# Kernel optimization log

Measured on AMD Instinct MI355X. Metric: run time of the kernel, lower is better.

Reference implementation:

```python
import jax, jax.numpy as jnp
import numpy as np

BN_EPS = 1e-5
STRIDE = 4
K_NEAREST = 16


def _fps(xyz, m):
    """Farthest point sampling. xyz: [n,3] -> indices [m] (seeded at point 0)."""
    n = xyz.shape[0]

    def body(i, state):
        dist, idxs, last = state
        d = jnp.sum((xyz - xyz[last]) ** 2, axis=-1)
        dist = jnp.minimum(dist, d)
        nxt = jnp.argmax(dist).astype(jnp.int32)
        return dist, idxs.at[i].set(nxt), nxt

    init = (jnp.full((n,), 1e10, xyz.dtype), jnp.zeros((m,), jnp.int32), jnp.int32(0))
    _, idxs, _ = jax.lax.fori_loop(1, m, body, init)
    return idxs


def _knn(q, x, k):
    """q: [m,3] queries, x: [n,3] points -> [m,k] nearest-neighbor indices."""
    d = jnp.sum((q[:, None, :] - x[None, :, :]) ** 2, axis=-1)  # [m,n]
    _, idx = jax.lax.top_k(-d, k)
    return idx


def setup_inputs() -> dict:
    key = jax.random.key(0)
    k0, k1, k2 = jax.random.split(key, 3)
    B, N, IN_CH, OUT_CH = 4, 8192, 64, 128
    events = jax.random.uniform(k0, (B, N, 4), dtype=jnp.float32)  # xyz in [0,1) + time
    features = jax.random.normal(k1, (B, N, IN_CH), dtype=jnp.float32)
    W = jax.random.normal(k2, (4 + IN_CH, OUT_CH), dtype=jnp.float32) / np.float32(np.sqrt(4 + IN_CH))
    b = jnp.zeros((OUT_CH,), jnp.float32)
    gamma = jnp.ones((OUT_CH,), jnp.float32)
    beta = jnp.zeros((OUT_CH,), jnp.float32)
    return dict(events=events, features=features, W=W, b=b, gamma=gamma, beta=beta)


def reference(events, features, W, b, gamma, beta):
    B, N, _ = events.shape
    m = N // STRIDE  # down_offsets = offsets // stride with equal-size samples
    xyz = events[..., :3]
    xyz_c = jax.lax.stop_gradient(xyz)  # indices are non-differentiable

    # farthest point sampling per cloud -> [B, m]
    down_idx = jax.vmap(lambda p: _fps(p, m))(xyz_c)
    down_xyz = jnp.take_along_axis(xyz_c, down_idx[..., None], axis=1)  # [B,m,3]
    # k nearest neighbors of each sampled point -> [B, m, K]
    idx = jax.vmap(lambda q, x: _knn(q, x, K_NEAREST))(down_xyz, xyz_c)

    down_events = jnp.take_along_axis(events, down_idx[..., None], axis=1)  # [B,m,4]
    grouped_events = jax.vmap(lambda e, i: e[i])(events, idx)               # [B,m,K,4]
    grouped_events_norm = grouped_events - down_events[:, :, None, :]
    grouped_features = jax.vmap(lambda f, i: f[i])(features, idx)           # [B,m,K,in_ch]
    g = jnp.concatenate([grouped_events_norm, grouped_features], axis=-1)   # [B,m,K,4+in_ch]

    # Linear -> BatchNorm1d (training batch stats over all points & neighbors) -> ReLU
    h = jnp.einsum('bmkc,cd->bmkd', g, W) + b
    mu = jnp.mean(h, axis=(0, 1, 2))
    var = jnp.var(h, axis=(0, 1, 2))
    h = (h - mu) * jax.lax.rsqrt(var + BN_EPS) * gamma + beta
    h = jax.nn.relu(h)

    down_features = jnp.max(h, axis=2)  # max-pool over K neighbors -> [B,m,out_ch]
    return down_events, down_features
```

## Files before the change

### kernel.cpp

```cpp
#include <hip/hip_runtime.h>

#define N_PTS 8192
#define M_PTS 2048
#define K_NN 16
#define IN_CH 64
#define G_CH 68
#define OUT_CH 128
#define KCAP 128

__device__ __forceinline__ float subrn(float a, float b) {
    float r; asm("v_sub_f32 %0, %1, %2" : "=v"(r) : "v"(a), "v"(b)); return r;
}
__device__ __forceinline__ float mulrn(float a, float b) {
    float r; asm("v_mul_f32 %0, %1, %2" : "=v"(r) : "v"(a), "v"(b)); return r;
}
__device__ __forceinline__ float addrn(float a, float b) {
    float r; asm("v_add_f32 %0, %1, %2" : "=v"(r) : "v"(a), "v"(b)); return r;
}
__device__ __forceinline__ float sqdist_rn(float ax, float ay, float az,
                                           float bx, float by, float bz) {
    float dx = subrn(ax, bx);
    float dy = subrn(ay, by);
    float dz = subrn(az, bz);
    return addrn(addrn(mulrn(dx, dx), mulrn(dy, dy)), mulrn(dz, dz));
}

typedef float v2f __attribute__((ext_vector_type(2)));
__device__ __forceinline__ v2f pk_add(v2f a, v2f b) {
    v2f r; asm("v_pk_add_f32 %0, %1, %2" : "=v"(r) : "v"(a), "v"(b)); return r;
}
__device__ __forceinline__ v2f pk_mul(v2f a, v2f b) {
    v2f r; asm("v_pk_mul_f32 %0, %1, %2" : "=v"(r) : "v"(a), "v"(b)); return r;
}

template <int CTRL>
__device__ __forceinline__ float movdpp_f(float x) {
    int r = __builtin_amdgcn_mov_dpp(__float_as_int(x), CTRL, 0xf, 0xf, true);
    return __int_as_float(r);
}
template <int CTRL>
__device__ __forceinline__ int movdpp_i(int x) {
    return __builtin_amdgcn_mov_dpp(x, CTRL, 0xf, 0xf, true);
}
template <int CTRL, int RM>
__device__ __forceinline__ float dppmaxf_m(float x) {
    int r = __builtin_amdgcn_update_dpp(0, __float_as_int(x), CTRL, RM, 0xf, false);
    return fmaxf(x, __int_as_float(r));
}
__device__ __forceinline__ float wave_max64(float x) {
    x = fmaxf(x, movdpp_f<0xB1>(x));
    x = fmaxf(x, movdpp_f<0x4E>(x));
    x = fmaxf(x, movdpp_f<0x141>(x));
    x = fmaxf(x, movdpp_f<0x140>(x));
    x = dppmaxf_m<0x142, 0xa>(x);
    x = dppmaxf_m<0x143, 0xc>(x);
    return x;
}
__device__ __forceinline__ float group8_max(float x) {
    x = fmaxf(x, movdpp_f<0xB1>(x));
    x = fmaxf(x, movdpp_f<0x4E>(x));
    x = fmaxf(x, movdpp_f<0x141>(x));
    return x;
}
__device__ __forceinline__ int group8_min_i(int x) {
    x = min(x, movdpp_i<0xB1>(x));
    x = min(x, movdpp_i<0x4E>(x));
    x = min(x, movdpp_i<0x141>(x));
    return x;
}

__global__ __launch_bounds__(512) void fps_kernel(const float4* __restrict__ events4,
                                                  int* __restrict__ down_idx,
                                                  float4* __restrict__ out_de) {
    extern __shared__ char smem[];
    float*  rv   = (float*)smem;
    int*    wsl  = (int*)(smem + 32);
    int*    ssel = (int*)(smem + 64);
    float4* spt  = (float4*)(smem + 64 + 4 * M_PTS);

    const int b = blockIdx.x;
    const int tid = threadIdx.x;
    const int wave = tid >> 6;
    const int lane = tid & 63;
    const float4* ev = events4 + (size_t)b * N_PTS;

    for (int i = tid; i < N_PTS; i += 512) spt[i] = ev[i];
    if (tid == 0) ssel[0] = 0;
    __syncthreads();

    v2f px[8], py[8], pz[8];
    float dist[16];
#pragma unroll
    for (int pp = 0; pp < 8; ++pp) {
        float4 f0 = spt[tid * 16 + 2 * pp];
        float4 f1 = spt[tid * 16 + 2 * pp + 1];
        px[pp] = (v2f){f0.x, f1.x};
        py[pp] = (v2f){f0.y, f1.y};
        pz[pp] = (v2f){f0.z, f1.z};
        dist[2 * pp] = 1e10f; dist[2 * pp + 1] = 1e10f;
    }

    int last = 0;
    for (int i = 1; i < M_PTS; ++i) {
        float4 L = spt[last];
        const float nlx = -L.x, nly = -L.y, nlz = -L.z;
        const v2f nx2 = (v2f){nlx, nlx};
        const v2f ny2 = (v2f){nly, nly};
        const v2f nz2 = (v2f){nlz, nlz};
#pragma unroll
        for (int pp = 0; pp < 8; ++pp) {
            v2f dx = pk_add(px[pp], nx2);
            v2f dy = pk_add(py[pp], ny2);
            v2f dz = pk_add(pz[pp], nz2);
            v2f s  = pk_add(pk_add(pk_mul(dx, dx), pk_mul(dy, dy)), pk_mul(dz, dz));
            dist[2 * pp]     = fminf(dist[2 * pp],     s.x);
            dist[2 * pp + 1] = fminf(dist[2 * pp + 1], s.y);
        }
        float m0 = fmaxf(dist[0], dist[1]),  m1 = fmaxf(dist[2], dist[3]);
        float m2 = fmaxf(dist[4], dist[5]),  m3 = fmaxf(dist[6], dist[7]);
        float m4 = fmaxf(dist[8], dist[9]),  m5 = fmaxf(dist[10], dist[11]);
        float m6 = fmaxf(dist[12], dist[13]), m7 = fmaxf(dist[14], dist[15]);
        m0 = fmaxf(m0, m1); m2 = fmaxf(m2, m3); m4 = fmaxf(m4, m5); m6 = fmaxf(m6, m7);
        float bd = fmaxf(fmaxf(m0, m2), fmaxf(m4, m6));

        float wm = wave_max64(bd);
        if (lane == 63) rv[wave] = wm;
        __syncthreads();
        float bm = group8_max(rv[lane & 7]);

        bool cand = (bd == bm);
        unsigned long long mask = __ballot(cand);
        if (lane == 0) wsl[wave] = 0x7fffffff;
        if (mask != 0ULL) {
            int fl = (int)__ffsll((long long)mask) - 1;
            if (lane == fl) {
                int jm = 0;
#pragma unroll
                for (int j = 15; j >= 0; --j) if (dist[j] == bd) jm = j;
                wsl[wave] = tid * 16 + jm;
            }
        }
        __syncthreads();
        int winner = group8_min_i(wsl[lane & 7]);
        if (tid == 0) ssel[i] = winner;
        last = winner;
    }
    __syncthreads();

    for (int i = tid; i < M_PTS; i += 512) {
        int s = ssel[i];
        down_idx[b * M_PTS + i] = s;
        out_de[(size_t)b * M_PTS + i] = spt[s];
    }
}

__global__ __launch_bounds__(256) void knn_kernel(const float4* __restrict__ events4,
                                                  const int* __restrict__ down_idx,
                                                  int* __restrict__ knn_idx) {
    extern __shared__ char smem[];
    float* sx   = (float*)smem;
    float* sy   = sx + N_PTS;
    float* sz   = sy + N_PTS;
    float* cd   = sz + N_PTS;
    int*   ci   = (int*)(cd + 32 * KCAP);
    int*   scnt = (int*)(ci + 32 * KCAP);

    const int b    = blockIdx.x >> 6;
    const int qg   = blockIdx.x & 63;
    const int tid  = threadIdx.x;
    const int ql   = tid >> 3;
    const int part = tid & 7;

    const float4* ev = events4 + (size_t)b * N_PTS;
    for (int i = tid; i < N_PTS; i += 256) {
        float4 e = ev[i];
        sx[i] = e.x; sy[i] = e.y; sz[i] = e.z;
    }
    if (tid < 32) scnt[tid] = 0;
    __syncthreads();

    const int q  = qg * 32 + ql;
    const int qi = down_idx[b * M_PTS + q];
    const float qx = sx[qi], qy = sy[qi], qz = sz[qi];

    float m1 = 1e30f, m2 = 1e30f;
    for (int i = 0; i < N_PTS / 8; ++i) {
        const int p = i * 8 + part;
        float d = sqdist_rn(sx[p], sy[p], sz[p], qx, qy, qz);
        float lo = fminf(m1, d);
        m2 = fminf(m2, fmaxf(m1, d));
        m1 = lo;
    }
    const float T = group8_max(m2);

    for (int i = 0; i < N_PTS / 8; ++i) {
        const int p = i * 8 + part;
        float d = sqdist_rn(sx[p], sy[p], sz[p], qx, qy, qz);
        if (d <= T) {
            int pos = atomicAdd(&scnt[ql], 1);
            if (pos < KCAP) { cd[ql * KCAP + pos] = d; ci[ql * KCAP + pos] = p; }
        }
    }
    __syncthreads();

    if (part == 0) {
        float nd[16]; int ni[16];
#pragma unroll
        for (int j = 0; j < 16; ++j) { nd[j] = 1e30f; ni[j] = 0x7fffffff; }
        float wmax = 1e30f; int widx = 0x7fffffff; int wslot = 0;
        const int n = scnt[ql];
        const int lim = (n <= KCAP) ? n : 0;
        for (int t = 0; t < lim; ++t) {
            float d = cd[ql * KCAP + t];
            int   p = ci[ql * KCAP + t];
            if (d < wmax || (d == wmax && p < widx)) {
#pragma unroll
                for (int j = 0; j < 16; ++j) if (j == wslot) { nd[j] = d; ni[j] = p; }
                float m_ = -1.0f; int mix_ = -1; int ms_ = 0;
#pragma unroll
                for (int j = 0; j < 16; ++j)
                    if (nd[j] > m_ || (nd[j] == m_ && ni[j] > mix_)) { m_ = nd[j]; mix_ = ni[j]; ms_ = j; }
                wmax = m_; widx = mix_; wslot = ms_;
            }
        }
        if (n > KCAP) {
            for (int p = 0; p < N_PTS; ++p) {
                float d = sqdist_rn(sx[p], sy[p], sz[p], qx, qy, qz);
                if (d < wmax || (d == wmax && p < widx)) {
#pragma unroll
                    for (int j = 0; j < 16; ++j) if (j == wslot) { nd[j] = d; ni[j] = p; }
                    float m_ = -1.0f; int mix_ = -1; int ms_ = 0;
#pragma unroll
                    for (int j = 0; j < 16; ++j)
                        if (nd[j] > m_ || (nd[j] == m_ && ni[j] > mix_)) { m_ = nd[j]; mix_ = ni[j]; ms_ = j; }
                    wmax = m_; widx = mix_; wslot = ms_;
                }
            }
        }
        int* out = knn_idx + ((size_t)(b * M_PTS + q)) * K_NN;
#pragma unroll
        for (int j = 0; j < 16; ++j) out[j] = ni[j];
    }
}

__global__ __launch_bounds__(256) void gmm_kernel(const float* __restrict__ events,
                                                  const float* __restrict__ features,
                                                  const float* __restrict__ W,
                                                  const float* __restrict__ bias,
                                                  const int* __restrict__ knn_idx,
                                                  const float* __restrict__ de,
                                                  float* __restrict__ hmax_g,
                                                  float* __restrict__ hmin_g,
                                                  float* __restrict__ gsum,
                                                  float* __restrict__ gsq) {
    __shared__ __align__(16) float sg[16 * G_CH];
    __shared__ float scomb[2 * OUT_CH];

    const int b   = blockIdx.x >> 7;
    const int qg  = blockIdx.x & 127;
    const int tid = threadIdx.x;
    const int d   = tid & 127;
    const int kh  = tid >> 7;

    float w[G_CH];
#pragma unroll
    for (int c = 0; c < G_CH; ++c) w[c] = W[c * OUT_CH + d];
    const float breg = bias[d];

    float ssum = 0.f, ssq = 0.f;
    const float4* sg4 = (const float4*)sg;

    for (int qq = 0; qq < 16; ++qq) {
        const int q = qg * 16 + qq;
        const int base = b * M_PTS + q;
        for (int j = tid; j < 16 * G_CH; j += 256) {
            int k = j / G_CH;
            int c = j - k * G_CH;
            int nb = knn_idx[base * K_NN + k];
            float v;
            if (c < 4) v = events[((size_t)(b * N_PTS + nb)) * 4 + c] - de[(size_t)base * 4 + c];
            else       v = features[((size_t)(b * N_PTS + nb)) * IN_CH + (c - 4)];
            sg[j] = v;
        }
        __syncthreads();

        float hmax = -1e30f, hmin = 1e30f;
#pragma unroll
        for (int k2 = 0; k2 < 8; ++k2) {
            const int k = kh * 8 + k2;
            float acc = breg;
#pragma unroll
            for (int c4 = 0; c4 < 17; ++c4) {
                float4 g = sg4[k * 17 + c4];
                acc = fmaf(g.x, w[4 * c4 + 0], acc);
                acc = fmaf(g.y, w[4 * c4 + 1], acc);
                acc = fmaf(g.z, w[4 * c4 + 2], acc);
                acc = fmaf(g.w, w[4 * c4 + 3], acc);
            }
            hmax = fmaxf(hmax, acc);
            hmin = fminf(hmin, acc);
            ssum += acc;
            ssq = fmaf(acc, acc, ssq);
        }
        if (kh == 1) { scomb[d] = hmax; scomb[OUT_CH + d] = hmin; }
        __syncthreads();
        if (kh == 0) {
            hmax = fmaxf(hmax, scomb[d]);
            hmin = fminf(hmin, scomb[OUT_CH + d]);
            hmax_g[(size_t)base * OUT_CH + d] = hmax;
            hmin_g[(size_t)base * OUT_CH + d] = hmin;
        }
        __syncthreads();
    }
    if (kh == 1) { scomb[d] = ssum; scomb[OUT_CH + d] = ssq; }
    __syncthreads();
    if (kh == 0) {
        atomicAdd(&gsum[d], ssum + scomb[d]);
        atomicAdd(&gsq[d],  ssq  + scomb[OUT_CH + d]);
    }
}

__global__ __launch_bounds__(256) void fin_kernel(const float* __restrict__ hmax_g,
                                                  const float* __restrict__ hmin_g,
                                                  const float* __restrict__ gsum,
                                                  const float* __restrict__ gsq,
                                                  const float* __restrict__ gamma,
                                                  const float* __restrict__ beta,
                                                  float* __restrict__ out) {
    const size_t e = (size_t)blockIdx.x * 256 + threadIdx.x;
    const int d = (int)(e & 127);
    const float inv_cnt = 1.0f / 131072.0f;
    float mu  = gsum[d] * inv_cnt;
    float var = gsq[d] * inv_cnt - mu * mu;
    float a   = gamma[d] * rsqrtf(var + 1e-5f);
    float sh  = fmaf(-mu, a, beta[d]);
    float hv  = (a >= 0.f) ? hmax_g[e] : hmin_g[e];
    float r   = fmaf(a, hv, sh);
    out[32768 + e] = r > 0.f ? r : 0.f;
}

extern "C" void kernel_launch(void* const* d_in, const int* in_sizes, int n_in,
                              void* d_out, int out_size, void* d_ws, size_t ws_size,
                              hipStream_t stream) {
    const float* events   = (const float*)d_in[0];
    const float* features = (const float*)d_in[1];
    const float* W        = (const float*)d_in[2];
    const float* bias     = (const float*)d_in[3];
    const float* gamma    = (const float*)d_in[4];
    const float* beta     = (const float*)d_in[5];
    float* out = (float*)d_out;
    char* ws = (char*)d_ws;

    int*   down_idx = (int*)ws;
    int*   knn_idx  = (int*)(ws + 32768);
    float* gsum     = (float*)(ws + 32768 + 524288);
    float* gsq      = gsum + OUT_CH;
    float* hmaxg    = (float*)(ws + 558080);
    float* hming    = hmaxg + (size_t)4 * M_PTS * OUT_CH;

    (void)hipMemsetAsync(gsum, 0, 2 * OUT_CH * sizeof(float), stream);

    const size_t fps_lds = 64 + 4 * M_PTS + (size_t)N_PTS * sizeof(float4);
    fps_kernel<<<4, 512, fps_lds, stream>>>((const float4*)events, down_idx, (float4*)out);

    const size_t knn_lds = (size_t)3 * N_PTS * sizeof(float)
                         + (size_t)32 * KCAP * 8 + 128;
    knn_kernel<<<256, 256, knn_lds, stream>>>((const float4*)events, down_idx, knn_idx);

    gmm_kernel<<<512, 256, 0, stream>>>(events, features, W, bias, knn_idx, out,
                                        hmaxg, hming, gsum, gsq);

    fin_kernel<<<4096, 256, 0, stream>>>(hmaxg, hming, gsum, gsq, gamma, beta, out);
}
```

Before: 2.443 ms.

## Streamline FPS argmax with LDS atomicMin and vectorize kNN/gather loads

The FPS loop replaces the ballot, per-wave slot write and second DPP min-reduction with a single LDS atomicMin into a double-buffered winner slot. Each thread now owns strided points instead of contiguous ones, so the lowest index still wins ties. kNN packs x,y into float2 in LDS so each distance needs one fewer LDS load, and the gmm gather now moves float4 chunks instead of scalars. The FPS change is meant to shorten the latency-bound serial loop, which dominates runtime, at the cost of atomic contention when several points tie.

New measurement: 2.427 ms. About the same (-0.7%).

```diff
diff --git a/kernel.cpp b/kernel.cpp
--- a/kernel.cpp
+++ b/kernel.cpp
@@ -37,10 +37,6 @@
 __device__ __forceinline__ float movdpp_f(float x) {
     int r = __builtin_amdgcn_mov_dpp(__float_as_int(x), CTRL, 0xf, 0xf, true);
     return __int_as_float(r);
-}
-template <int CTRL>
-__device__ __forceinline__ int movdpp_i(int x) {
-    return __builtin_amdgcn_mov_dpp(x, CTRL, 0xf, 0xf, true);
 }
 template <int CTRL, int RM>
 __device__ __forceinline__ float dppmaxf_m(float x) {
@@ -62,12 +58,6 @@
     x = fmaxf(x, movdpp_f<0x141>(x));
     return x;
 }
-__device__ __forceinline__ int group8_min_i(int x) {
-    x = min(x, movdpp_i<0xB1>(x));
-    x = min(x, movdpp_i<0x4E>(x));
-    x = min(x, movdpp_i<0x141>(x));
-    return x;
-}
 
 __global__ __launch_bounds__(512) void fps_kernel(const float4* __restrict__ events4,
                                                   int* __restrict__ down_idx,
@@ -85,15 +75,15 @@
     const float4* ev = events4 + (size_t)b * N_PTS;
 
     for (int i = tid; i < N_PTS; i += 512) spt[i] = ev[i];
-    if (tid == 0) ssel[0] = 0;
+    if (tid == 0) { ssel[0] = 0; wsl[0] = 0x7fffffff; wsl[1] = 0x7fffffff; }
     __syncthreads();
 
     v2f px[8], py[8], pz[8];
     float dist[16];
 #pragma unroll
     for (int pp = 0; pp < 8; ++pp) {
-        float4 f0 = spt[tid * 16 + 2 * pp];
-        float4 f1 = spt[tid * 16 + 2 * pp + 1];
+        float4 f0 = spt[(2 * pp) * 512 + tid];
+        float4 f1 = spt[(2 * pp + 1) * 512 + tid];
         px[pp] = (v2f){f0.x, f1.x};
         py[pp] = (v2f){f0.y, f1.y};
         pz[pp] = (v2f){f0.z, f1.z};
@@ -116,34 +106,27 @@
             dist[2 * pp]     = fminf(dist[2 * pp],     s.x);
             dist[2 * pp + 1] = fminf(dist[2 * pp + 1], s.y);
         }
-        float m0 = fmaxf(dist[0], dist[1]),  m1 = fmaxf(dist[2], dist[3]);
-        float m2 = fmaxf(dist[4], dist[5]),  m3 = fmaxf(dist[6], dist[7]);
-        float m4 = fmaxf(dist[8], dist[9]),  m5 = fmaxf(dist[10], dist[11]);
-        float m6 = fmaxf(dist[12], dist[13]), m7 = fmaxf(dist[14], dist[15]);
-        m0 = fmaxf(m0, m1); m2 = fmaxf(m2, m3); m4 = fmaxf(m4, m5); m6 = fmaxf(m6, m7);
-        float bd = fmaxf(fmaxf(m0, m2), fmaxf(m4, m6));
+        float t0[8];
+#pragma unroll
+        for (int j = 0; j < 8; ++j) t0[j] = fmaxf(dist[2 * j], dist[2 * j + 1]);
+#pragma unroll
+        for (int j = 0; j < 4; ++j) t0[j] = fmaxf(t0[2 * j], t0[2 * j + 1]);
+        float bd = fmaxf(fmaxf(t0[0], t0[1]), fmaxf(t0[2], t0[3]));
 
         float wm = wave_max64(bd);
         if (lane == 63) rv[wave] = wm;
         __syncthreads();
         float bm = group8_max(rv[lane & 7]);
 
-        bool cand = (bd == bm);
-        unsigned long long mask = __ballot(cand);
-        if (lane == 0) wsl[wave] = 0x7fffffff;
-        if (mask != 0ULL) {
-            int fl = (int)__ffsll((long long)mask) - 1;
-            if (lane == fl) {
-                int jm = 0;
-#pragma unroll
-                for (int j = 15; j >= 0; --j) if (dist[j] == bd) jm = j;
-                wsl[wave] = tid * 16 + jm;
-            }
-        }
-        __syncthreads();
-        int winner = group8_min_i(wsl[lane & 7]);
-        if (tid == 0) ssel[i] = winner;
-        last = winner;
+        if (bd == bm) {
+            int jm = 0;
+#pragma unroll
+            for (int j = 15; j >= 0; --j) if (dist[j] == bd) jm = j;
+            atomicMin(&wsl[i & 1], jm * 512 + tid);
+        }
+        __syncthreads();
+        last = wsl[i & 1];
+        if (tid == 0) { ssel[i] = last; wsl[(i + 1) & 1] = 0x7fffffff; }
     }
     __syncthreads();
 
@@ -158,12 +141,11 @@
                                                   const int* __restrict__ down_idx,
                                                   int* __restrict__ knn_idx) {
     extern __shared__ char smem[];
-    float* sx   = (float*)smem;
-    float* sy   = sx + N_PTS;
-    float* sz   = sy + N_PTS;
-    float* cd   = sz + N_PTS;
-    int*   ci   = (int*)(cd + 32 * KCAP);
-    int*   scnt = (int*)(ci + 32 * KCAP);
+    float2* sxy  = (float2*)smem;
+    float*  sz   = (float*)(smem + N_PTS * 8);
+    float*  cd   = sz + N_PTS;
+    int*    ci   = (int*)(cd + 32 * KCAP);
+    int*    scnt = (int*)(ci + 32 * KCAP);
 
     const int b    = blockIdx.x >> 6;
     const int qg   = blockIdx.x & 63;
@@ -174,19 +156,21 @@
     const float4* ev = events4 + (size_t)b * N_PTS;
     for (int i = tid; i < N_PTS; i += 256) {
         float4 e = ev[i];
-        sx[i] = e.x; sy[i] = e.y; sz[i] = e.z;
+        sxy[i] = (float2){e.x, e.y}; sz[i] = e.z;
     }
     if (tid < 32) scnt[tid] = 0;
     __syncthreads();
 
     const int q  = qg * 32 + ql;
     const int qi = down_idx[b * M_PTS + q];
-    const float qx = sx[qi], qy = sy[qi], qz = sz[qi];
+    const float2 qxy = sxy[qi];
+    const float qx = qxy.x, qy = qxy.y, qz = sz[qi];
 
     float m1 = 1e30f, m2 = 1e30f;
     for (int i = 0; i < N_PTS / 8; ++i) {
         const int p = i * 8 + part;
-        float d = sqdist_rn(sx[p], sy[p], sz[p], qx, qy, qz);
+        float2 pxy = sxy[p];
+        float d = sqdist_rn(pxy.x, pxy.y, sz[p], qx, qy, qz);
         float lo = fminf(m1, d);
         m2 = fminf(m2, fmaxf(m1, d));
         m1 = lo;
@@ -195,7 +179,8 @@
 
     for (int i = 0; i < N_PTS / 8; ++i) {
         const int p = i * 8 + part;
-        float d = sqdist_rn(sx[p], sy[p], sz[p], qx, qy, qz);
+        float2 pxy = sxy[p];
+        float d = sqdist_rn(pxy.x, pxy.y, sz[p], qx, qy, qz);
         if (d <= T) {
             int pos = atomicAdd(&scnt[ql], 1);
             if (pos < KCAP) { cd[ql * KCAP + pos] = d; ci[ql * KCAP + pos] = p; }
@@ -225,7 +210,8 @@
         }
         if (n > KCAP) {
             for (int p = 0; p < N_PTS; ++p) {
-                float d = sqdist_rn(sx[p], sy[p], sz[p], qx, qy, qz);
+                float2 pxy = sxy[p];
+                float d = sqdist_rn(pxy.x, pxy.y, sz[p], qx, qy, qz);
                 if (d < wmax || (d == wmax && p < widx)) {
 #pragma unroll
                     for (int j = 0; j < 16; ++j) if (j == wslot) { nd[j] = d; ni[j] = p; }
@@ -243,12 +229,12 @@
     }
 }
 
-__global__ __launch_bounds__(256) void gmm_kernel(const float* __restrict__ events,
-                                                  const float* __restrict__ features,
+__global__ __launch_bounds__(256) void gmm_kernel(const float4* __restrict__ events4,
+                                                  const float4* __restrict__ feat4,
                                                   const float* __restrict__ W,
                                                   const float* __restrict__ bias,
                                                   const int* __restrict__ knn_idx,
-                                                  const float* __restrict__ de,
+                                                  const float4* __restrict__ de4,
                                                   float* __restrict__ hmax_g,
                                                   float* __restrict__ hmin_g,
                                                   float* __restrict__ gsum,
@@ -268,19 +254,25 @@
     const float breg = bias[d];
 
     float ssum = 0.f, ssq = 0.f;
-    const float4* sg4 = (const float4*)sg;
+    const float4* sg4r = (const float4*)sg;
+    float4* sg4w = (float4*)sg;
 
     for (int qq = 0; qq < 16; ++qq) {
         const int q = qg * 16 + qq;
         const int base = b * M_PTS + q;
-        for (int j = tid; j < 16 * G_CH; j += 256) {
-            int k = j / G_CH;
-            int c = j - k * G_CH;
+        for (int j4 = tid; j4 < 16 * 17; j4 += 256) {
+            int k = j4 / 17;
+            int c4 = j4 - k * 17;
             int nb = knn_idx[base * K_NN + k];
-            float v;
-            if (c < 4) v = events[((size_t)(b * N_PTS + nb)) * 4 + c] - de[(size_t)base * 4 + c];
-            else       v = features[((size_t)(b * N_PTS + nb)) * IN_CH + (c - 4)];
-            sg[j] = v;
+            float4 v;
+            if (c4 == 0) {
+                float4 e = events4[(size_t)b * N_PTS + nb];
+                float4 d0 = de4[base];
+                v = (float4){e.x - d0.x, e.y - d0.y, e.z - d0.z, e.w - d0.w};
+            } else {
+                v = feat4[((size_t)(b * N_PTS + nb)) * 16 + (c4 - 1)];
+            }
+            sg4w[j4] = v;
         }
         __syncthreads();
 
@@ -291,7 +283,7 @@
             float acc = breg;
 #pragma unroll
             for (int c4 = 0; c4 < 17; ++c4) {
-                float4 g = sg4[k * 17 + c4];
+                float4 g = sg4r[k * 17 + c4];
                 acc = fmaf(g.x, w[4 * c4 + 0], acc);
                 acc = fmaf(g.y, w[4 * c4 + 1], acc);
                 acc = fmaf(g.z, w[4 * c4 + 2], acc);
@@ -363,11 +355,12 @@
     const size_t fps_lds = 64 + 4 * M_PTS + (size_t)N_PTS * sizeof(float4);
     fps_kernel<<<4, 512, fps_lds, stream>>>((const float4*)events, down_idx, (float4*)out);
 
-    const size_t knn_lds = (size_t)3 * N_PTS * sizeof(float)
+    const size_t knn_lds = (size_t)N_PTS * 8 + (size_t)N_PTS * 4
                          + (size_t)32 * KCAP * 8 + 128;
     knn_kernel<<<256, 256, knn_lds, stream>>>((const float4*)events, down_idx, knn_idx);
 
-    gmm_kernel<<<512, 256, 0, stream>>>(events, features, W, bias, knn_idx, out,
+    gmm_kernel<<<512, 256, 0, stream>>>((const float4*)events, (const float4*)features,
+                                        W, bias, knn_idx, (const float4*)out,
                                         hmaxg, hming, gsum, gsq);
 
     fin_kernel<<<4096, 256, 0, stream>>>(hmaxg, hming, gsum, gsq, gamma, beta, out);
```
